# Performance work log

Measured on AMD Instinct MI355X. Metric: run time of the kernel, lower is better.

The kernel has to match this reference:

```python
import jax, jax.numpy as jnp
import numpy as np

B, S, D_IN, D = 2, 4096, 1024, 64  # batch, seq_len, input_dim, head dim d


def setup_inputs() -> dict:
    key = jax.random.key(0)
    k1, k2, k3, k4 = jax.random.split(key, 4)
    X = jax.random.normal(k1, (B, S, D_IN), dtype=jnp.float32)
    W_q = jax.random.normal(k2, (D_IN, 2 * D), dtype=jnp.float32) / np.sqrt(D_IN)
    W_k = jax.random.normal(k3, (D_IN, 2 * D), dtype=jnp.float32) / np.sqrt(D_IN)
    W_v = jax.random.normal(k4, (D_IN, 2 * D), dtype=jnp.float32) / np.sqrt(D_IN)
    lam = jnp.float32(0.8)
    return {"X": X, "W_q": W_q, "W_k": W_k, "W_v": W_v, "lam": lam}


def reference(X, W_q, W_k, W_v, lam):
    d = W_q.shape[-1] // 2
    Q = X @ W_q  # [B, S, 2d]
    K = X @ W_k  # [B, S, 2d]
    V = X @ W_v  # [B, S, 2d]
    Q1, Q2 = Q[..., :d], Q[..., d:]
    K1, K2 = K[..., :d], K[..., d:]
    s = 1.0 / jnp.sqrt(jnp.float32(d))
    A1 = jnp.einsum("bqd,bkd->bqk", Q1, K1) * s  # [B, S, S]
    A2 = jnp.einsum("bqd,bkd->bqk", Q2, K2) * s  # [B, S, S]
    P = jax.nn.softmax(A1, axis=-1) - lam * jax.nn.softmax(A2, axis=-1)
    return jnp.einsum("bqk,bkv->bqv", P, V)  # [B, S, 2d]
```

## Files before the change

### kernel.cpp

```cpp
#include <hip/hip_runtime.h>
#include <hip/hip_bf16.h>

typedef float f32x4 __attribute__((ext_vector_type(4)));
typedef float f32x16 __attribute__((ext_vector_type(16)));
typedef short bf16x8 __attribute__((ext_vector_type(8)));

#define MFMA16(A,B,C) __builtin_amdgcn_mfma_f32_16x16x32_bf16(A,B,C,0,0,0)
#define MFMA32(A,B,C) __builtin_amdgcn_mfma_f32_32x32x16_bf16(A,B,C,0,0,0)

__device__ __forceinline__ unsigned short f2bf(float f) {
    union { float f; unsigned u; } x; x.f = f;
    return (unsigned short)((x.u + 0x7FFFu + ((x.u >> 16) & 1u)) >> 16);
}

__device__ __forceinline__ float bf2f(unsigned short u) {
    union { unsigned u; float f; } x; x.u = ((unsigned)u) << 16; return x.f;
}

__device__ __forceinline__ unsigned fbits(float f) {
    union { float f; unsigned u; } x; x.f = f; return x.u;
}

__device__ __forceinline__ f32x16 zero16() {
    f32x16 z;
#pragma unroll
    for (int i = 0; i < 16; ++i) z[i] = 0.f;
    return z;
}

typedef const __attribute__((address_space(1))) unsigned int* as1_t;
typedef __attribute__((address_space(3))) unsigned int* as3_t;
__device__ __forceinline__ void gl_lds16(const unsigned short* g, unsigned short* l) {
    __builtin_amdgcn_global_load_lds((as1_t)g, (as3_t)l, 16, 0, 0);
}

__global__ __launch_bounds__(256) void prep(const float* __restrict__ Wq,
        const float* __restrict__ Wk, const float* __restrict__ Wv,
        unsigned short* __restrict__ WT) {
    int w = blockIdx.x % 3;
    int kt = blockIdx.x / 3;
    const float* src = (w == 0) ? Wq : (w == 1) ? Wk : Wv;
    int k0 = kt * 32;
#pragma unroll
    for (int j = 0; j < 16; ++j) {
        int idx = threadIdx.x + j * 256;
        int r = idx >> 7, c = idx & 127;
        float v = src[(size_t)(k0 + r) * 128 + c];
        WT[(size_t)(w * 128 + c) * 1024 + k0 + r] = f2bf(v);
    }
}

__global__ __launch_bounds__(256) void proj(const float* __restrict__ Xf,
        const unsigned short* __restrict__ WT, unsigned short* __restrict__ Qc,
        unsigned short* __restrict__ Kc, unsigned short* __restrict__ VT) {
    int tid = threadIdx.x;
    int w = tid >> 6, lane = tid & 63;
    int lr = lane & 15, lg = lane >> 4;
    int wr = w >> 1, wc = w & 1;
    int m0 = blockIdx.x * 64;
    int n0 = blockIdx.y * 96;

    __shared__ __align__(16) unsigned short Ab[3][64 * 64];
    __shared__ __align__(16) unsigned short Bb[3][96 * 64];

    f32x4 acc[2][3];
#pragma unroll
    for (int i = 0; i < 2; ++i)
#pragma unroll
        for (int j = 0; j < 3; ++j) acc[i][j] = f32x4{0.f,0.f,0.f,0.f};

    int srow = lane >> 3;
    int sunit = lane & 7;
    const unsigned short* bSrc = WT + (size_t)(n0 + srow) * 1024 + sunit * 8;

    float4 aReg[4];
    auto A_LOAD = [&](int st) {
        int kk = st * 64;
#pragma unroll
        for (int i = 0; i < 4; ++i) {
            int f = tid + i * 256;
            int row = f >> 4, c4 = f & 15;
            aReg[i] = *(const float4*)(Xf + (size_t)(m0 + row) * 1024 + kk + c4 * 4);
        }
    };
    auto A_WRITE = [&](unsigned short* ad) {
#pragma unroll
        for (int i = 0; i < 4; ++i) {
            int f = tid + i * 256;
            int row = f >> 4, c4 = f & 15;
            ushort4 pk;
            pk.x = f2bf(aReg[i].x); pk.y = f2bf(aReg[i].y);
            pk.z = f2bf(aReg[i].z); pk.w = f2bf(aReg[i].w);
            *(ushort4*)(ad + row * 64 + c4 * 4) = pk;
        }
    };
    auto B_STAGE = [&](unsigned short* bd, int st) {
        int kk = st * 64;
#pragma unroll
        for (int i = 0; i < 3; ++i) {
            int blk = w * 3 + i;
            gl_lds16(bSrc + (size_t)blk * 8 * 1024 + kk, bd + blk * 512);
        }
    };

    unsigned short *a0 = Ab[0], *a1 = Ab[1], *a2 = Ab[2];
    unsigned short *b0 = Bb[0], *b1 = Bb[1], *b2 = Bb[2];
    A_LOAD(0); B_STAGE(b0, 0);
    A_WRITE(a0);
    A_LOAD(1); B_STAGE(b1, 1);
    A_WRITE(a1);

    for (int st = 0; st < 16; ++st) {
        if (st < 15) asm volatile("s_waitcnt vmcnt(3) lgkmcnt(0)" ::: "memory");
        else         asm volatile("s_waitcnt vmcnt(0) lgkmcnt(0)" ::: "memory");
        __builtin_amdgcn_sched_barrier(0);
        __builtin_amdgcn_s_barrier();
        __builtin_amdgcn_sched_barrier(0);
        if (st + 2 < 16) { A_LOAD(st + 2); B_STAGE(b2, st + 2); }

        const unsigned short* ab = a0;
        const unsigned short* bb = b0;
#pragma unroll
        for (int ksub = 0; ksub < 2; ++ksub) {
            int ko = ksub * 32 + lg * 8;
            bf16x8 af[2], bf[3];
#pragma unroll
            for (int mt = 0; mt < 2; ++mt)
                af[mt] = *(const bf16x8*)(ab + (wr * 32 + mt * 16 + lr) * 64 + ko);
#pragma unroll
            for (int nt = 0; nt < 3; ++nt)
                bf[nt] = *(const bf16x8*)(bb + (wc * 48 + nt * 16 + lr) * 64 + ko);
#pragma unroll
            for (int mt = 0; mt < 2; ++mt)
#pragma unroll
                for (int nt = 0; nt < 3; ++nt)
                    acc[mt][nt] = MFMA16(af[mt], bf[nt], acc[mt][nt]);
        }
        if (st + 2 < 16) A_WRITE(a2);

        unsigned short* t;
        t = a0; a0 = a1; a1 = a2; a2 = t;
        t = b0; b0 = b1; b1 = b2; b2 = t;
    }

    int b = m0 >> 12;
    int sbase = (m0 & 4095) + wr * 32;
#pragma unroll
    for (int nt = 0; nt < 3; ++nt) {
        int gcol = n0 + wc * 48 + nt * 16 + lr;
        int tensor = gcol >> 7;
#pragma unroll
        for (int mt = 0; mt < 2; ++mt) {
            int sloc = sbase + mt * 16 + 4 * lg;
            if (tensor == 2) {
                int vcol = gcol & 127;
                int slocV = (sloc & ~15) | (((lg & 1) << 3) | ((lg >> 1) << 2));
                ushort4 pk;
                pk.x = f2bf(acc[mt][nt][0]); pk.y = f2bf(acc[mt][nt][1]);
                pk.z = f2bf(acc[mt][nt][2]); pk.w = f2bf(acc[mt][nt][3]);
                *(ushort4*)(VT + (size_t)(b * 128 + vcol) * 4096 + slocV) = pk;
            } else {
                int within = gcol & 127;
                int comp = within >> 6;
                int col64 = within & 63;
                float sc = (tensor == 0) ? 0.1803368801f : 1.0f;
                unsigned short* dst = (tensor == 0) ? Qc : Kc;
                size_t rowb = (size_t)(comp * 2 + b) * 4096 + sloc;
#pragma unroll
                for (int r = 0; r < 4; ++r)
                    dst[(rowb + r) * 64 + col64] = f2bf(acc[mt][nt][r] * sc);
            }
        }
    }
}

__global__ __launch_bounds__(256, 2) void attn(const unsigned short* __restrict__ Qc,
        const unsigned short* __restrict__ Kc, const unsigned short* __restrict__ VT,
        unsigned short* __restrict__ Opart, float* __restrict__ Lpart) {
    int tid = threadIdx.x;
    int wave = tid >> 6, lane = tid & 63;
    int l31 = lane & 31, hi = lane >> 5;
    int x7 = l31 & 7;
    int b = blockIdx.y;
    int comp = blockIdx.z >> 2, split = blockIdx.z & 3;
    int q0 = blockIdx.x * 128 + wave * 32;
    int kstart = split * 1024;

    __shared__ __align__(16) unsigned short kb3[3][64 * 64];
    __shared__ __align__(16) unsigned short vb3[3][128 * 64];

    const unsigned short* Qp = Qc + ((size_t)(comp * 2 + b) * 4096 + q0 + l31) * 64 + hi * 8;
    bf16x8 qB0 = *(const bf16x8*)(Qp);
    bf16x8 qB1 = *(const bf16x8*)(Qp + 16);
    bf16x8 qB2 = *(const bf16x8*)(Qp + 32);
    bf16x8 qB3 = *(const bf16x8*)(Qp + 48);

    f32x16 o[4];
#pragma unroll
    for (int i = 0; i < 4; ++i) o[i] = zero16();
    float lsum = 0.f;

    const unsigned short* kSrc = Kc + ((size_t)(comp * 2 + b) * 4096 + kstart
                                       + wave * 8 + (lane >> 3)) * 64
                                    + ((lane & 7) ^ (lane >> 3)) * 8;
    const unsigned short* vSrc = VT + ((size_t)b * 128 + (tid >> 3)) * 4096
                                    + kstart + ((lane & 7) ^ (lane >> 3)) * 8;

    auto STAGE = [&](unsigned short* kd, unsigned short* vd, int it) {
        const unsigned short* ks = kSrc + (size_t)it * 4096;
        gl_lds16(ks,        kd + wave * 512);
        gl_lds16(ks + 2048, kd + 2048 + wave * 512);
        const unsigned short* vs = vSrc + it * 64;
#pragma unroll
        for (int ri = 0; ri < 4; ++ri)
            gl_lds16(vs + (size_t)ri * 32 * 4096, vd + ri * 2048 + wave * 512);
    };

    unsigned short *k0 = kb3[0], *k1 = kb3[1], *k2 = kb3[2];
    unsigned short *v0 = vb3[0], *v1 = vb3[1], *v2 = vb3[2];
    STAGE(k0, v0, 0);
    STAGE(k1, v1, 1);

    for (int it = 0; it < 16; ++it) {
        if (it < 15) asm volatile("s_waitcnt vmcnt(6)" ::: "memory");
        else         asm volatile("s_waitcnt vmcnt(0)" ::: "memory");
        __builtin_amdgcn_sched_barrier(0);
        __builtin_amdgcn_s_barrier();
        __builtin_amdgcn_sched_barrier(0);
        if (it + 2 < 16) STAGE(k2, v2, it + 2);

        const unsigned short* kb = k0;
        const unsigned short* vb = v0;

        f32x16 st0 = zero16(), st1 = zero16();
        __builtin_amdgcn_s_setprio(1);
#pragma unroll
        for (int j = 0; j < 4; ++j) {
            int ku = ((j * 2 + hi) ^ x7) * 8;
            bf16x8 kA0 = *(const bf16x8*)(kb + l31 * 64 + ku);
            bf16x8 kA1 = *(const bf16x8*)(kb + (32 + l31) * 64 + ku);
            bf16x8 qj = (j == 0) ? qB0 : (j == 1) ? qB1 : (j == 2) ? qB2 : qB3;
            st0 = MFMA32(kA0, qj, st0);
            st1 = MFMA32(kA1, qj, st1);
        }
        __builtin_amdgcn_s_setprio(0);

        union W4 { unsigned u[4]; bf16x8 v; };
        W4 wA0, wB0, wA1, wB1;
#pragma unroll
        for (int i2 = 0; i2 < 4; ++i2) {
            float a0 = __builtin_amdgcn_exp2f(st0[2 * i2]);
            float a1 = __builtin_amdgcn_exp2f(st0[2 * i2 + 1]);
            float a2 = __builtin_amdgcn_exp2f(st0[8 + 2 * i2]);
            float a3 = __builtin_amdgcn_exp2f(st0[9 + 2 * i2]);
            float b0 = __builtin_amdgcn_exp2f(st1[2 * i2]);
            float b1 = __builtin_amdgcn_exp2f(st1[2 * i2 + 1]);
            float b2 = __builtin_amdgcn_exp2f(st1[8 + 2 * i2]);
            float b3 = __builtin_amdgcn_exp2f(st1[9 + 2 * i2]);
            lsum += (a0 + a1) + (a2 + a3) + (b0 + b1) + (b2 + b3);
            wA0.u[i2] = __builtin_amdgcn_perm(fbits(a1), fbits(a0), 0x07060302);
            wB0.u[i2] = __builtin_amdgcn_perm(fbits(a3), fbits(a2), 0x07060302);
            wA1.u[i2] = __builtin_amdgcn_perm(fbits(b1), fbits(b0), 0x07060302);
            wB1.u[i2] = __builtin_amdgcn_perm(fbits(b3), fbits(b2), 0x07060302);
        }

        __builtin_amdgcn_s_setprio(1);
#pragma unroll
        for (int vt = 0; vt < 4; ++vt) {
            const unsigned short* vrow = vb + (vt * 32 + l31) * 64;
            o[vt] = MFMA32(wA0.v, *(const bf16x8*)(vrow + ((0 + hi) ^ x7) * 8), o[vt]);
            o[vt] = MFMA32(wB0.v, *(const bf16x8*)(vrow + ((2 + hi) ^ x7) * 8), o[vt]);
            o[vt] = MFMA32(wA1.v, *(const bf16x8*)(vrow + ((4 + hi) ^ x7) * 8), o[vt]);
            o[vt] = MFMA32(wB1.v, *(const bf16x8*)(vrow + ((6 + hi) ^ x7) * 8), o[vt]);
        }
        __builtin_amdgcn_s_setprio(0);

        unsigned short* t;
        t = k0; k0 = k1; k1 = k2; k2 = t;
        t = v0; v0 = v1; v1 = v2; v2 = t;
    }

    int base = (b * 2 + comp) * 4 + split;
    unsigned short* op = Opart + (size_t)base * 4096 * 128;
#pragma unroll
    for (int vt = 0; vt < 4; ++vt)
#pragma unroll
        for (int r = 0; r < 16; ++r) {
            int qr = (r & 3) + 8 * (r >> 2) + 4 * hi;
            op[(size_t)(q0 + qr) * 128 + vt * 32 + l31] = f2bf(o[vt][r]);
        }
    float ls = lsum + __shfl_xor(lsum, 32, 64);
    if (hi == 0)
        Lpart[(size_t)base * 4096 + q0 + l31] = ls;
}

__global__ __launch_bounds__(256) void combine(const unsigned short* __restrict__ Opart,
        const float* __restrict__ Lpart, const float* __restrict__ lamp,
        float* __restrict__ out) {
    float lam = lamp[0];
    int i = blockIdx.x * 256 + threadIdx.x;
    int row = i >> 5;
    int c4  = i & 31;
    int b = row >> 12, q = row & 4095;

    float l1 = 0.f, l2 = 0.f;
#pragma unroll
    for (int s = 0; s < 4; ++s) {
        l1 += Lpart[((size_t)((b * 2 + 0) * 4 + s)) * 4096 + q];
        l2 += Lpart[((size_t)((b * 2 + 1) * 4 + s)) * 4096 + q];
    }
    float rl1 = 1.0f / l1, rl2 = 1.0f / l2;

    size_t qoff = (size_t)q * 128 + c4 * 4;
    float a0 = 0.f, a1 = 0.f, a2 = 0.f, a3 = 0.f;
    float c0 = 0.f, c1 = 0.f, c2 = 0.f, c3 = 0.f;
#pragma unroll
    for (int s = 0; s < 4; ++s) {
        ushort4 p1 = *(const ushort4*)(Opart + (size_t)((b * 2 + 0) * 4 + s) * 4096 * 128 + qoff);
        ushort4 p2 = *(const ushort4*)(Opart + (size_t)((b * 2 + 1) * 4 + s) * 4096 * 128 + qoff);
        a0 += bf2f(p1.x); a1 += bf2f(p1.y); a2 += bf2f(p1.z); a3 += bf2f(p1.w);
        c0 += bf2f(p2.x); c1 += bf2f(p2.y); c2 += bf2f(p2.z); c3 += bf2f(p2.w);
    }
    float4 r;
    r.x = a0 * rl1 - lam * c0 * rl2;
    r.y = a1 * rl1 - lam * c1 * rl2;
    r.z = a2 * rl1 - lam * c2 * rl2;
    r.w = a3 * rl1 - lam * c3 * rl2;
    ((float4*)out)[i] = r;
}

extern "C" void kernel_launch(void* const* d_in, const int* in_sizes, int n_in,
                              void* d_out, int out_size, void* d_ws, size_t ws_size,
                              hipStream_t stream) {
    const float* X   = (const float*)d_in[0];
    const float* Wq  = (const float*)d_in[1];
    const float* Wk  = (const float*)d_in[2];
    const float* Wv  = (const float*)d_in[3];
    const float* lam = (const float*)d_in[4];
    float* out = (float*)d_out;

    char* ws = (char*)d_ws;
    unsigned short* Qc = (unsigned short*)(ws);
    unsigned short* Kc = (unsigned short*)(ws + 2097152);
    unsigned short* VT = (unsigned short*)(ws + 4194304);
    unsigned short* WT = (unsigned short*)(ws + 6291456);
    unsigned short* Opart = (unsigned short*)(ws + 6291456);
    float* Lpart = (float*)(ws + 23068672);

    prep<<<dim3(96), dim3(256), 0, stream>>>(Wq, Wk, Wv, WT);
    proj<<<dim3(128, 4), dim3(256), 0, stream>>>(X, WT, Qc, Kc, VT);
    attn<<<dim3(32, 2, 8), dim3(256), 0, stream>>>(Qc, Kc, VT, Opart, Lpart);
    combine<<<dim3(1024), dim3(256), 0, stream>>>(Opart, Lpart, lam, out);
}
```

Measured before the change: 66.84 us.

## Split attention keys eight ways with 32-key tiles and new V LDS layout

The attention kernel now splits the key range into 8 chunks instead of 4, processes 32 keys per iteration instead of 64, and stores V tiles in a chunked LDS layout without swizzle. Launch bounds ask for 3 blocks per CU, and the grid doubles to 1024 blocks. The aim is more parallelism and occupancy, trading larger LDS tile reuse for more blocks. In exchange, the partial-output buffer doubles and the combine kernel reads twice as many partials, adding global memory traffic.

```diff
diff --git a/kernel.cpp b/kernel.cpp
--- a/kernel.cpp
+++ b/kernel.cpp
@@ -174,7 +174,7 @@
     }
 }
 
-__global__ __launch_bounds__(256, 2) void attn(const unsigned short* __restrict__ Qc,
+__global__ __launch_bounds__(256, 3) void attn(const unsigned short* __restrict__ Qc,
         const unsigned short* __restrict__ Kc, const unsigned short* __restrict__ VT,
         unsigned short* __restrict__ Opart, float* __restrict__ Lpart) {
     int tid = threadIdx.x;
@@ -182,12 +182,12 @@
     int l31 = lane & 31, hi = lane >> 5;
     int x7 = l31 & 7;
     int b = blockIdx.y;
-    int comp = blockIdx.z >> 2, split = blockIdx.z & 3;
+    int comp = blockIdx.z >> 3, split = blockIdx.z & 7;
     int q0 = blockIdx.x * 128 + wave * 32;
-    int kstart = split * 1024;
-
-    __shared__ __align__(16) unsigned short kb3[3][64 * 64];
-    __shared__ __align__(16) unsigned short vb3[3][128 * 64];
+    int kstart = split * 512;
+
+    __shared__ __align__(16) unsigned short kb3[3][32 * 64];
+    __shared__ __align__(16) unsigned short vb3[3][4 * 128 * 8];
 
     const unsigned short* Qp = Qc + ((size_t)(comp * 2 + b) * 4096 + q0 + l31) * 64 + hi * 8;
     bf16x8 qB0 = *(const bf16x8*)(Qp);
@@ -203,17 +203,14 @@
     const unsigned short* kSrc = Kc + ((size_t)(comp * 2 + b) * 4096 + kstart
                                        + wave * 8 + (lane >> 3)) * 64
                                     + ((lane & 7) ^ (lane >> 3)) * 8;
-    const unsigned short* vSrc = VT + ((size_t)b * 128 + (tid >> 3)) * 4096
-                                    + kstart + ((lane & 7) ^ (lane >> 3)) * 8;
+    const unsigned short* vSrc = VT + ((size_t)b * 128 + lane) * 4096
+                                    + kstart + wave * 8;
 
     auto STAGE = [&](unsigned short* kd, unsigned short* vd, int it) {
-        const unsigned short* ks = kSrc + (size_t)it * 4096;
-        gl_lds16(ks,        kd + wave * 512);
-        gl_lds16(ks + 2048, kd + 2048 + wave * 512);
-        const unsigned short* vs = vSrc + it * 64;
-#pragma unroll
-        for (int ri = 0; ri < 4; ++ri)
-            gl_lds16(vs + (size_t)ri * 32 * 4096, vd + ri * 2048 + wave * 512);
+        gl_lds16(kSrc + (size_t)it * 2048, kd + wave * 512);
+        const unsigned short* vs = vSrc + it * 32;
+        gl_lds16(vs,                      vd + wave * 1024);
+        gl_lds16(vs + (size_t)64 * 4096,  vd + wave * 1024 + 512);
     };
 
     unsigned short *k0 = kb3[0], *k1 = kb3[1], *k2 = kb3[2];
@@ -222,7 +219,7 @@
     STAGE(k1, v1, 1);
 
     for (int it = 0; it < 16; ++it) {
-        if (it < 15) asm volatile("s_waitcnt vmcnt(6)" ::: "memory");
+        if (it < 15) asm volatile("s_waitcnt vmcnt(3)" ::: "memory");
         else         asm volatile("s_waitcnt vmcnt(0)" ::: "memory");
         __builtin_amdgcn_sched_barrier(0);
         __builtin_amdgcn_s_barrier();
@@ -232,46 +229,36 @@
         const unsigned short* kb = k0;
         const unsigned short* vb = v0;
 
-        f32x16 st0 = zero16(), st1 = zero16();
+        f32x16 st0 = zero16();
         __builtin_amdgcn_s_setprio(1);
 #pragma unroll
         for (int j = 0; j < 4; ++j) {
             int ku = ((j * 2 + hi) ^ x7) * 8;
             bf16x8 kA0 = *(const bf16x8*)(kb + l31 * 64 + ku);
-            bf16x8 kA1 = *(const bf16x8*)(kb + (32 + l31) * 64 + ku);
             bf16x8 qj = (j == 0) ? qB0 : (j == 1) ? qB1 : (j == 2) ? qB2 : qB3;
             st0 = MFMA32(kA0, qj, st0);
-            st1 = MFMA32(kA1, qj, st1);
         }
         __builtin_amdgcn_s_setprio(0);
 
         union W4 { unsigned u[4]; bf16x8 v; };
-        W4 wA0, wB0, wA1, wB1;
+        W4 wA0, wB0;
 #pragma unroll
         for (int i2 = 0; i2 < 4; ++i2) {
             float a0 = __builtin_amdgcn_exp2f(st0[2 * i2]);
             float a1 = __builtin_amdgcn_exp2f(st0[2 * i2 + 1]);
             float a2 = __builtin_amdgcn_exp2f(st0[8 + 2 * i2]);
             float a3 = __builtin_amdgcn_exp2f(st0[9 + 2 * i2]);
-            float b0 = __builtin_amdgcn_exp2f(st1[2 * i2]);
-            float b1 = __builtin_amdgcn_exp2f(st1[2 * i2 + 1]);
-            float b2 = __builtin_amdgcn_exp2f(st1[8 + 2 * i2]);
-            float b3 = __builtin_amdgcn_exp2f(st1[9 + 2 * i2]);
-            lsum += (a0 + a1) + (a2 + a3) + (b0 + b1) + (b2 + b3);
+            lsum += (a0 + a1) + (a2 + a3);
             wA0.u[i2] = __builtin_amdgcn_perm(fbits(a1), fbits(a0), 0x07060302);
             wB0.u[i2] = __builtin_amdgcn_perm(fbits(a3), fbits(a2), 0x07060302);
-            wA1.u[i2] = __builtin_amdgcn_perm(fbits(b1), fbits(b0), 0x07060302);
-            wB1.u[i2] = __builtin_amdgcn_perm(fbits(b3), fbits(b2), 0x07060302);
         }
 
         __builtin_amdgcn_s_setprio(1);
 #pragma unroll
         for (int vt = 0; vt < 4; ++vt) {
-            const unsigned short* vrow = vb + (vt * 32 + l31) * 64;
-            o[vt] = MFMA32(wA0.v, *(const bf16x8*)(vrow + ((0 + hi) ^ x7) * 8), o[vt]);
-            o[vt] = MFMA32(wB0.v, *(const bf16x8*)(vrow + ((2 + hi) ^ x7) * 8), o[vt]);
-            o[vt] = MFMA32(wA1.v, *(const bf16x8*)(vrow + ((4 + hi) ^ x7) * 8), o[vt]);
-            o[vt] = MFMA32(wB1.v, *(const bf16x8*)(vrow + ((6 + hi) ^ x7) * 8), o[vt]);
+            const unsigned short* vrow = vb + (vt * 32 + l31) * 8;
+            o[vt] = MFMA32(wA0.v, *(const bf16x8*)(vrow + (0 + hi) * 1024), o[vt]);
+            o[vt] = MFMA32(wB0.v, *(const bf16x8*)(vrow + (2 + hi) * 1024), o[vt]);
         }
         __builtin_amdgcn_s_setprio(0);
 
@@ -280,7 +267,7 @@
         t = v0; v0 = v1; v1 = v2; v2 = t;
     }
 
-    int base = (b * 2 + comp) * 4 + split;
+    int base = (b * 2 + comp) * 8 + split;
     unsigned short* op = Opart + (size_t)base * 4096 * 128;
 #pragma unroll
     for (int vt = 0; vt < 4; ++vt)
@@ -305,9 +292,9 @@
 
     float l1 = 0.f, l2 = 0.f;
 #pragma unroll
-    for (int s = 0; s < 4; ++s) {
-        l1 += Lpart[((size_t)((b * 2 + 0) * 4 + s)) * 4096 + q];
-        l2 += Lpart[((size_t)((b * 2 + 1) * 4 + s)) * 4096 + q];
+    for (int s = 0; s < 8; ++s) {
+        l1 += Lpart[((size_t)((b * 2 + 0) * 8 + s)) * 4096 + q];
+        l2 += Lpart[((size_t)((b * 2 + 1) * 8 + s)) * 4096 + q];
     }
     float rl1 = 1.0f / l1, rl2 = 1.0f / l2;
 
@@ -315,9 +302,9 @@
     float a0 = 0.f, a1 = 0.f, a2 = 0.f, a3 = 0.f;
     float c0 = 0.f, c1 = 0.f, c2 = 0.f, c3 = 0.f;
 #pragma unroll
-    for (int s = 0; s < 4; ++s) {
-        ushort4 p1 = *(const ushort4*)(Opart + (size_t)((b * 2 + 0) * 4 + s) * 4096 * 128 + qoff);
-        ushort4 p2 = *(const ushort4*)(Opart + (size_t)((b * 2 + 1) * 4 + s) * 4096 * 128 + qoff);
+    for (int s = 0; s < 8; ++s) {
+        ushort4 p1 = *(const ushort4*)(Opart + (size_t)((b * 2 + 0) * 8 + s) * 4096 * 128 + qoff);
+        ushort4 p2 = *(const ushort4*)(Opart + (size_t)((b * 2 + 1) * 8 + s) * 4096 * 128 + qoff);
         a0 += bf2f(p1.x); a1 += bf2f(p1.y); a2 += bf2f(p1.z); a3 += bf2f(p1.w);
         c0 += bf2f(p2.x); c1 += bf2f(p2.y); c2 += bf2f(p2.z); c3 += bf2f(p2.w);
     }
@@ -345,10 +332,10 @@
     unsigned short* VT = (unsigned short*)(ws + 4194304);
     unsigned short* WT = (unsigned short*)(ws + 6291456);
     unsigned short* Opart = (unsigned short*)(ws + 6291456);
-    float* Lpart = (float*)(ws + 23068672);
+    float* Lpart = (float*)(ws + 39845888);
 
     prep<<<dim3(96), dim3(256), 0, stream>>>(Wq, Wk, Wv, WT);
     proj<<<dim3(128, 4), dim3(256), 0, stream>>>(X, WT, Qc, Kc, VT);
-    attn<<<dim3(32, 2, 8), dim3(256), 0, stream>>>(Qc, Kc, VT, Opart, Lpart);
+    attn<<<dim3(32, 2, 16), dim3(256), 0, stream>>>(Qc, Kc, VT, Opart, Lpart);
     combine<<<dim3(1024), dim3(256), 0, stream>>>(Opart, Lpart, lam, out);
 }
```

After: 72.07 us. 7.8% more time.
